# Optimization experiments

Hardware: AMD Instinct MI355X
Metric: run time of the kernel (lower is better)

## Reference

```python
import jax, jax.numpy as jnp
import numpy as np

N_NODES = 50000
N_EDGES = 300000
D = 256  # node/edge feature dim; MLP input = 3*D = 768


def setup_inputs() -> dict:
    key = jax.random.key(0)
    ks = jax.random.split(key, 5)
    x_node = jax.random.normal(ks[0], (N_NODES, D), dtype=jnp.float32)
    x_edge = jax.random.normal(ks[1], (N_EDGES, D), dtype=jnp.float32)
    edge_index = jax.random.randint(ks[2], (2, N_EDGES), 0, N_NODES, dtype=jnp.int64)
    # MLP params: Linear(3*D, D) -> ReLU -> Linear(D, D)
    W1 = jax.random.normal(ks[3], (3 * D, D), dtype=jnp.float32) * (1.0 / np.sqrt(3 * D))
    b1 = jnp.zeros((D,), dtype=jnp.float32)
    W2 = jax.random.normal(ks[4], (D, D), dtype=jnp.float32) * (1.0 / np.sqrt(D))
    b2 = jnp.zeros((D,), dtype=jnp.float32)
    return {"x_node": x_node, "x_edge": x_edge, "edge_index": edge_index,
            "W1": W1, "b1": b1, "W2": W2, "b2": b2}


def reference(x_node, x_edge, edge_index, W1, b1, W2, b2):
    # gather src/dst node feats and concat with edge feats: [E, 3*D]
    src = x_node[edge_index[0]]
    dst = x_node[edge_index[1]]
    h = jnp.concatenate([src, dst, x_edge], axis=1)
    # MLP (custom_func): Linear -> ReLU -> Linear
    h = jax.nn.relu(h @ W1 + b1)
    x_edge_ = h @ W2 + b2
    return x_edge_
```

## Files before the change

### kernel.cpp

```cpp
#include <hip/hip_runtime.h>


typedef __attribute__((ext_vector_type(8))) short short8;
typedef __attribute__((ext_vector_type(4))) float f32x4;
typedef __attribute__((address_space(1))) unsigned int* gp1_t;
typedef __attribute__((address_space(3))) unsigned int* lp3_t;

#define LDO 260

__device__ __forceinline__ unsigned short f2b(float f) {
  unsigned int u = __float_as_uint(f);
  return (unsigned short)((u + 0x7FFFu + ((u >> 16) & 1u)) >> 16);
}
__device__ __forceinline__ unsigned int f2b2(float lo, float hi) {
  return (unsigned int)f2b(lo) | ((unsigned int)f2b(hi) << 16);
}
__device__ __forceinline__ float b2f(unsigned int u) {
  return __uint_as_float((u & 0xffffu) << 16);
}
__device__ __forceinline__ void gload16(const void* g, void* l) {
  __builtin_amdgcn_global_load_lds((gp1_t)g, (lp3_t)l, 16, 0, 0);
}

__global__ void prep_w_kernel(const float* __restrict__ w,
                              unsigned short* __restrict__ wp, int total) {
  int i = blockIdx.x * 256 + threadIdx.x;
  if (i >= total) return;
  int step = i >> 14;
  int rem = i & 16383;
  int n = rem >> 6;
  int s = (rem >> 3) & 7;
  int j = i & 7;
  int k = step * 64 + (((s ^ (n & 7)) << 3) | j);
  wp[i] = f2b(w[(size_t)k * 256 + n]);
}

__global__ __launch_bounds__(512) void node_p_kernel(
    const float* __restrict__ xnode, const unsigned short* __restrict__ wtab,
    unsigned short* __restrict__ Pbase, int NN) {
  __shared__ __align__(16) char smem[65536];

  const int t = threadIdx.x, w = t >> 6, l = t & 63;
  const int lr = l & 15, lk = l >> 4;
  const int wr = w >> 2, wc = w & 3;
  const int nbase = blockIdx.x * 256;
  const char* wt = (const char*)wtab + blockIdx.y * 131072;
  unsigned short* P = Pbase + (size_t)blockIdx.y * NN * 256;

  const int r2 = t >> 1;
  int row2 = nbase + r2;
  if (row2 >= NN) row2 = NN - 1;

  f32x4 acc[8][4];
#pragma unroll
  for (int i = 0; i < 8; ++i)
#pragma unroll
    for (int j = 0; j < 4; ++j) acc[i][j] = (f32x4)0.0f;

  auto stageA = [&](int s, int buf) {
    const int rb = r2 & 7;
    float4 v[8];
#pragma unroll
    for (int jj = 0; jj < 4; ++jj) {
      const int j = (t & 1) * 4 + jj;
      const float* p = xnode + (size_t)row2 * 256 + s * 64 + j * 8;
      v[2 * jj] = ((const float4*)p)[0];
      v[2 * jj + 1] = ((const float4*)p)[1];
    }
#pragma unroll
    for (int jj = 0; jj < 4; ++jj) {
      const int j = (t & 1) * 4 + jj;
      uint4 u;
      u.x = f2b2(v[2 * jj].x, v[2 * jj].y);
      u.y = f2b2(v[2 * jj].z, v[2 * jj].w);
      u.z = f2b2(v[2 * jj + 1].x, v[2 * jj + 1].y);
      u.w = f2b2(v[2 * jj + 1].z, v[2 * jj + 1].w);
      *(uint4*)(smem + buf * 32768 + r2 * 128 + ((j ^ rb) << 4)) = u;
    }
  };

  stageA(0, 0);
  __syncthreads();
  for (int k = 0; k < 4; ++k) {
    if (k + 1 < 4) stageA(k + 1, (k + 1) & 1);
    const char* A = smem + (k & 1) * 32768;
    const char* wb = wt + k * 32768;
    __builtin_amdgcn_s_setprio(1);
#pragma unroll
    for (int ks = 0; ks < 2; ++ks) {
      short8 bf[4];
#pragma unroll
      for (int ni = 0; ni < 4; ++ni) {
        const int n = wc * 64 + ni * 16 + lr;
        bf[ni] = *(const short8*)(wb + n * 128 + (((ks * 4 + lk) ^ (n & 7)) << 4));
      }
#pragma unroll
      for (int mi = 0; mi < 8; ++mi) {
        const int m = wr * 128 + mi * 16 + lr;
        short8 af = *(const short8*)(A + m * 128 + (((ks * 4 + lk) ^ (m & 7)) << 4));
#pragma unroll
        for (int ni = 0; ni < 4; ++ni)
          acc[mi][ni] = __builtin_amdgcn_mfma_f32_16x16x32_bf16(
              af, bf[ni], acc[mi][ni], 0, 0, 0);
      }
    }
    __builtin_amdgcn_s_setprio(0);
    __syncthreads();
  }

#pragma unroll
  for (int mi = 0; mi < 8; ++mi)
#pragma unroll
    for (int r = 0; r < 4; ++r) {
      const int node = nbase + wr * 128 + mi * 16 + lk * 4 + r;
      if (node < NN) {
        uint2 o;
        o.x = f2b2(acc[mi][0][r], acc[mi][1][r]);
        o.y = f2b2(acc[mi][2][r], acc[mi][3][r]);
        *(uint2*)((char*)P + (size_t)node * 512 + lr * 32 + wc * 8) = o;
      }
    }
}

__global__ __launch_bounds__(512) void edge_mlp_p(
    const float* __restrict__ xedge, const int* __restrict__ eidx,
    const unsigned short* __restrict__ Ps, const unsigned short* __restrict__ Pd,
    const unsigned short* __restrict__ wt1ep, const float* __restrict__ b1,
    const unsigned short* __restrict__ wt2p, const float* __restrict__ b2,
    float* __restrict__ out, int E) {
  __shared__ __align__(16) char smem[133120];

  const int t = threadIdx.x, w = t >> 6, l = t & 63;
  const int lr = l & 15, lk = l >> 4;
  const int wr = w >> 2, wc = w & 3;
  const int ebase = blockIdx.x * 256;

  int* sIdx = (int*)(smem + 131072);
  int* dIdx = (int*)(smem + 131072 + 1024);
  {
    const int i = t & 255;
    int e = ebase + i;
    if (e >= E) e = E - 1;
    if (t < 256) sIdx[i] = eidx[e];
    else         dIdx[i] = eidx[(size_t)E + e];
  }

  const int r2 = t >> 1;
  int e2 = ebase + r2;
  if (e2 >= E) e2 = E - 1;

  f32x4 acc[8][4];
#pragma unroll
  for (int i = 0; i < 8; ++i)
#pragma unroll
    for (int j = 0; j < 4; ++j) acc[i][j] = (f32x4)0.0f;

  auto stageB = [&](int step, int buf) {
    const char* g = (const char*)wt1ep + (size_t)step * 32768 + (t << 4);
    char* d = smem + 65536 + buf * 32768 + (w << 10) + (l << 4);
#pragma unroll
    for (int q = 0; q < 4; ++q) gload16(g + q * 8192, d + q * 8192);
  };
  auto stageA = [&](int s, int buf) {
    const int rb = r2 & 7;
    float4 v[8];
#pragma unroll
    for (int jj = 0; jj < 4; ++jj) {
      const int j = (t & 1) * 4 + jj;
      const float* p = xedge + (size_t)e2 * 256 + s * 64 + j * 8;
      v[2 * jj] = ((const float4*)p)[0];
      v[2 * jj + 1] = ((const float4*)p)[1];
    }
#pragma unroll
    for (int jj = 0; jj < 4; ++jj) {
      const int j = (t & 1) * 4 + jj;
      uint4 u;
      u.x = f2b2(v[2 * jj].x, v[2 * jj].y);
      u.y = f2b2(v[2 * jj].z, v[2 * jj].w);
      u.z = f2b2(v[2 * jj + 1].x, v[2 * jj + 1].y);
      u.w = f2b2(v[2 * jj + 1].z, v[2 * jj + 1].w);
      *(uint4*)(smem + buf * 32768 + r2 * 128 + ((j ^ rb) << 4)) = u;
    }
  };
  auto compute = [&](int k) {
    const char* A = smem + (k & 1) * 32768;
    const char* B = smem + 65536 + (k & 1) * 32768;
    __builtin_amdgcn_s_setprio(1);
#pragma unroll
    for (int ks = 0; ks < 2; ++ks) {
      short8 bf[4];
#pragma unroll
      for (int ni = 0; ni < 4; ++ni) {
        const int n = wc * 64 + ni * 16 + lr;
        bf[ni] = *(const short8*)(B + n * 128 + (((ks * 4 + lk) ^ (n & 7)) << 4));
      }
#pragma unroll
      for (int mi = 0; mi < 8; ++mi) {
        const int m = wr * 128 + mi * 16 + lr;
        short8 af = *(const short8*)(A + m * 128 + (((ks * 4 + lk) ^ (m & 7)) << 4));
#pragma unroll
        for (int ni = 0; ni < 4; ++ni)
          acc[mi][ni] = __builtin_amdgcn_mfma_f32_16x16x32_bf16(
              af, bf[ni], acc[mi][ni], 0, 0, 0);
      }
    }
    __builtin_amdgcn_s_setprio(0);
  };

  stageA(0, 0);
  stageB(0, 0);
  __syncthreads();
  for (int k = 0; k < 4; ++k) {
    if (k + 1 < 4) {
      stageB(k + 1, (k + 1) & 1);
      stageA(k + 1, (k + 1) & 1);
    }
    compute(k);
    __syncthreads();
  }

  char* Hs = smem;
  float bias4[4];
#pragma unroll
  for (int ni = 0; ni < 4; ++ni) bias4[ni] = b1[wc * 64 + ni * 16 + lr];
#pragma unroll
  for (int mi = 0; mi < 8; ++mi) {
    uint2 pls[4], pld[4];
#pragma unroll
    for (int r = 0; r < 4; ++r) {
      const int m = wr * 128 + mi * 16 + lk * 4 + r;
      const int si = sIdx[m], di = dIdx[m];
      pls[r] = *(const uint2*)((const char*)Ps + (size_t)si * 512 + lr * 32 + wc * 8);
      pld[r] = *(const uint2*)((const char*)Pd + (size_t)di * 512 + lr * 32 + wc * 8);
    }
#pragma unroll
    for (int ni = 0; ni < 4; ++ni) {
      const int col = wc * 64 + ni * 16 + lr;
      const int cole = col & ~1;
      const int chunk = cole >> 3;
      const int cb = (cole & 6) * 2;
      float v[4], p[4];
#pragma unroll
      for (int r = 0; r < 4; ++r) {
        const unsigned us = (ni < 2) ? (pls[r].x >> (16 * ni)) : (pls[r].y >> (16 * (ni - 2)));
        const unsigned ud = (ni < 2) ? (pld[r].x >> (16 * ni)) : (pld[r].y >> (16 * (ni - 2)));
        float x = acc[mi][ni][r] + bias4[ni] + b2f(us) + b2f(ud);
        v[r] = x > 0.f ? x : 0.f;
        acc[mi][ni][r] = 0.f;
      }
#pragma unroll
      for (int r = 0; r < 4; ++r) p[r] = __shfl_xor(v[r], 1, 64);
      const int r0 = (lr & 1) ? 2 : 0;
#pragma unroll
      for (int rr = 0; rr < 2; ++rr) {
        const int r = r0 + rr;
        const int row = wr * 128 + mi * 16 + lk * 4 + r;
        const float lo = (lr & 1) ? p[r] : v[r];
        const float hi = (lr & 1) ? v[r] : p[r];
        *(unsigned int*)(Hs + row * 512 + ((chunk ^ (row & 7)) << 4) + cb) =
            f2b2(lo, hi);
      }
    }
  }
  __syncthreads();

  short8 bfA[4], bfB[4];
  auto loadB2 = [&](int pair, short8 (&bf)[4]) {
    const char* wb = (const char*)wt2p + (pair >> 1) * 32768;
    const int ksl = (pair & 1) * 4 + lk;
#pragma unroll
    for (int ni = 0; ni < 4; ++ni) {
      const int n = wc * 64 + ni * 16 + lr;
      bf[ni] = *(const short8*)(wb + n * 128 + ((ksl ^ (n & 7)) << 4));
    }
  };
  auto mfmaH = [&](int pair, short8 (&bf)[4]) {
    const int j = (pair >> 1) * 8 + (pair & 1) * 4 + lk;
    __builtin_amdgcn_s_setprio(1);
#pragma unroll
    for (int mi = 0; mi < 8; ++mi) {
      const int m = wr * 128 + mi * 16 + lr;
      short8 af = *(const short8*)(Hs + m * 512 + ((j ^ (m & 7)) << 4));
#pragma unroll
      for (int ni = 0; ni < 4; ++ni)
        acc[mi][ni] = __builtin_amdgcn_mfma_f32_16x16x32_bf16(
            af, bf[ni], acc[mi][ni], 0, 0, 0);
    }
    __builtin_amdgcn_s_setprio(0);
  };
  loadB2(0, bfA);
#pragma unroll
  for (int pair = 0; pair < 8; pair += 2) {
    if (pair + 1 < 8) loadB2(pair + 1, bfB);
    mfmaH(pair, bfA);
    if (pair + 2 < 8) loadB2(pair + 2, bfA);
    if (pair + 1 < 8) mfmaH(pair + 1, bfB);
  }

  float* outst = (float*)smem;
#pragma unroll
  for (int p = 0; p < 4; ++p) {
    __syncthreads();
    if (wr == (p >> 1)) {
#pragma unroll
      for (int ni = 0; ni < 4; ++ni) {
        const int col = wc * 64 + ni * 16 + lr;
        const float bias = b2[col];
#pragma unroll
        for (int mh = 0; mh < 4; ++mh) {
          const int mi = (p & 1) * 4 + mh;
#pragma unroll
          for (int r = 0; r < 4; ++r)
            outst[(mh * 16 + lk * 4 + r) * LDO + col] = acc[mi][ni][r] + bias;
        }
      }
    }
    __syncthreads();
#pragma unroll
    for (int it = 0; it < 8; ++it) {
      const int idx = it * 2048 + t * 4;
      const int lrow = idx >> 8;
      const int cc = idx & 255;
      const int grow = ebase + p * 64 + lrow;
      if (grow < E)
        *(float4*)(out + (size_t)grow * 256 + cc) =
            *(const float4*)(outst + lrow * LDO + cc);
    }
  }
}

__global__ __launch_bounds__(512) void edge_mlp_fb(
    const float* __restrict__ xnode, const float* __restrict__ xedge,
    const int* __restrict__ eidx,
    const unsigned short* __restrict__ wt1p, const float* __restrict__ b1,
    const unsigned short* __restrict__ wt2p, const float* __restrict__ b2,
    float* __restrict__ out, int E) {
  __shared__ __align__(16) char smem[131072];

  const int t = threadIdx.x, w = t >> 6, l = t & 63;
  const int lr = l & 15, lk = l >> 4;
  const int wr = w >> 2, wc = w & 3;
  const int ebase = blockIdx.x * 256;

  const int r2 = t >> 1;
  int e2 = ebase + r2;
  if (e2 >= E) e2 = E - 1;
  const int ns2 = eidx[e2], nd2 = eidx[(size_t)E + e2];

  f32x4 acc[8][4];
#pragma unroll
  for (int i = 0; i < 8; ++i)
#pragma unroll
    for (int j = 0; j < 4; ++j) acc[i][j] = (f32x4)0.0f;

  auto stageB = [&](int step, int buf) {
    const char* g = (const char*)wt1p + (size_t)step * 32768 + (t << 4);
    char* d = smem + 65536 + buf * 32768 + (w << 10) + (l << 4);
#pragma unroll
    for (int q = 0; q < 4; ++q) gload16(g + q * 8192, d + q * 8192);
  };
  auto stageA_f32 = [&](const float* base, int rowid, int coloff, int buf) {
    const int rb = r2 & 7;
    float4 v[8];
#pragma unroll
    for (int jj = 0; jj < 4; ++jj) {
      const int j = (t & 1) * 4 + jj;
      const float* p = base + (size_t)rowid * 256 + coloff + j * 8;
      v[2 * jj] = ((const float4*)p)[0];
      v[2 * jj + 1] = ((const float4*)p)[1];
    }
#pragma unroll
    for (int jj = 0; jj < 4; ++jj) {
      const int j = (t & 1) * 4 + jj;
      uint4 u;
      u.x = f2b2(v[2 * jj].x, v[2 * jj].y);
      u.y = f2b2(v[2 * jj].z, v[2 * jj].w);
      u.z = f2b2(v[2 * jj + 1].x, v[2 * jj + 1].y);
      u.w = f2b2(v[2 * jj + 1].z, v[2 * jj + 1].w);
      *(uint4*)(smem + buf * 32768 + r2 * 128 + ((j ^ rb) << 4)) = u;
    }
  };
  auto stageA = [&](int s, int buf) {
    if (s < 4)       stageA_f32(xnode, ns2, s * 64, buf);
    else if (s < 8)  stageA_f32(xnode, nd2, (s - 4) * 64, buf);
    else             stageA_f32(xedge, e2, (s - 8) * 64, buf);
  };
  auto compute = [&](int k) {
    const char* A = smem + (k & 1) * 32768;
    const char* B = smem + 65536 + (k & 1) * 32768;
    __builtin_amdgcn_s_setprio(1);
#pragma unroll
    for (int ks = 0; ks < 2; ++ks) {
      short8 bf[4];
#pragma unroll
      for (int ni = 0; ni < 4; ++ni) {
        const int n = wc * 64 + ni * 16 + lr;
        bf[ni] = *(const short8*)(B + n * 128 + (((ks * 4 + lk) ^ (n & 7)) << 4));
      }
#pragma unroll
      for (int mi = 0; mi < 8; ++mi) {
        const int m = wr * 128 + mi * 16 + lr;
        short8 af = *(const short8*)(A + m * 128 + (((ks * 4 + lk) ^ (m & 7)) << 4));
#pragma unroll
        for (int ni = 0; ni < 4; ++ni)
          acc[mi][ni] = __builtin_amdgcn_mfma_f32_16x16x32_bf16(
              af, bf[ni], acc[mi][ni], 0, 0, 0);
      }
    }
    __builtin_amdgcn_s_setprio(0);
  };

  stageA(0, 0);
  stageB(0, 0);
  __syncthreads();
  for (int k = 0; k < 12; ++k) {
    if (k + 1 < 12) {
      stageB(k + 1, (k + 1) & 1);
      stageA(k + 1, (k + 1) & 1);
    }
    compute(k);
    __syncthreads();
  }

  char* Hs = smem;
#pragma unroll
  for (int ni = 0; ni < 4; ++ni) {
    const int col = wc * 64 + ni * 16 + lr;
    const float bias = b1[col];
    const int cole = col & ~1;
    const int chunk = cole >> 3;
    const int cb = (cole & 6) * 2;
#pragma unroll
    for (int mi = 0; mi < 8; ++mi) {
      float v[4], p[4];
#pragma unroll
      for (int r = 0; r < 4; ++r) {
        float x = acc[mi][ni][r] + bias;
        v[r] = x > 0.f ? x : 0.f;
        acc[mi][ni][r] = 0.f;
      }
#pragma unroll
      for (int r = 0; r < 4; ++r) p[r] = __shfl_xor(v[r], 1, 64);
      const int r0 = (lr & 1) ? 2 : 0;
#pragma unroll
      for (int rr = 0; rr < 2; ++rr) {
        const int r = r0 + rr;
        const int row = wr * 128 + mi * 16 + lk * 4 + r;
        const float lo = (lr & 1) ? p[r] : v[r];
        const float hi = (lr & 1) ? v[r] : p[r];
        *(unsigned int*)(Hs + row * 512 + ((chunk ^ (row & 7)) << 4) + cb) =
            f2b2(lo, hi);
      }
    }
  }
  __syncthreads();

  short8 bfA[4], bfB[4];
  auto loadB2 = [&](int pair, short8 (&bf)[4]) {
    const char* wb = (const char*)wt2p + (pair >> 1) * 32768;
    const int ksl = (pair & 1) * 4 + lk;
#pragma unroll
    for (int ni = 0; ni < 4; ++ni) {
      const int n = wc * 64 + ni * 16 + lr;
      bf[ni] = *(const short8*)(wb + n * 128 + ((ksl ^ (n & 7)) << 4));
    }
  };
  auto mfmaH = [&](int pair, short8 (&bf)[4]) {
    const int j = (pair >> 1) * 8 + (pair & 1) * 4 + lk;
    __builtin_amdgcn_s_setprio(1);
#pragma unroll
    for (int mi = 0; mi < 8; ++mi) {
      const int m = wr * 128 + mi * 16 + lr;
      short8 af = *(const short8*)(Hs + m * 512 + ((j ^ (m & 7)) << 4));
#pragma unroll
      for (int ni = 0; ni < 4; ++ni)
        acc[mi][ni] = __builtin_amdgcn_mfma_f32_16x16x32_bf16(
            af, bf[ni], acc[mi][ni], 0, 0, 0);
    }
    __builtin_amdgcn_s_setprio(0);
  };
  loadB2(0, bfA);
#pragma unroll
  for (int pair = 0; pair < 8; pair += 2) {
    if (pair + 1 < 8) loadB2(pair + 1, bfB);
    mfmaH(pair, bfA);
    if (pair + 2 < 8) loadB2(pair + 2, bfA);
    if (pair + 1 < 8) mfmaH(pair + 1, bfB);
  }

  float* outst = (float*)smem;
#pragma unroll
  for (int p = 0; p < 4; ++p) {
    __syncthreads();
    if (wr == (p >> 1)) {
#pragma unroll
      for (int ni = 0; ni < 4; ++ni) {
        const int col = wc * 64 + ni * 16 + lr;
        const float bias = b2[col];
#pragma unroll
        for (int mh = 0; mh < 4; ++mh) {
          const int mi = (p & 1) * 4 + mh;
#pragma unroll
          for (int r = 0; r < 4; ++r)
            outst[(mh * 16 + lk * 4 + r) * LDO + col] = acc[mi][ni][r] + bias;
        }
      }
    }
    __syncthreads();
#pragma unroll
    for (int it = 0; it < 8; ++it) {
      const int idx = it * 2048 + t * 4;
      const int lrow = idx >> 8;
      const int cc = idx & 255;
      const int grow = ebase + p * 64 + lrow;
      if (grow < E)
        *(float4*)(out + (size_t)grow * 256 + cc) =
            *(const float4*)(outst + lrow * LDO + cc);
    }
  }
}

extern "C" void kernel_launch(void* const* d_in, const int* in_sizes, int n_in,
                              void* d_out, int out_size, void* d_ws, size_t ws_size,
                              hipStream_t stream) {
  const float* xnode = (const float*)d_in[0];
  const float* xedge = (const float*)d_in[1];
  const int* eidx = (const int*)d_in[2];
  const float* W1 = (const float*)d_in[3];
  const float* b1 = (const float*)d_in[4];
  const float* W2 = (const float*)d_in[5];
  const float* b2 = (const float*)d_in[6];
  float* out = (float*)d_out;

  const int NN = in_sizes[0] / 256;
  const int E = in_sizes[1] / 256;
  const int grid = (E + 255) / 256;

  char* ws = (char*)d_ws;
  const size_t need_new = 4 * 131072 + (size_t)2 * NN * 512;

  if (ws_size >= need_new) {
    unsigned short* wt1sp = (unsigned short*)ws;
    unsigned short* wt1dp = (unsigned short*)(ws + 131072);
    unsigned short* wt1ep = (unsigned short*)(ws + 262144);
    unsigned short* wt2p  = (unsigned short*)(ws + 393216);
    unsigned short* Ps    = (unsigned short*)(ws + 524288);
    unsigned short* Pd    = Ps + (size_t)NN * 256;

    prep_w_kernel<<<256, 256, 0, stream>>>(W1, wt1sp, 65536);
    prep_w_kernel<<<256, 256, 0, stream>>>(W1 + 65536, wt1dp, 65536);
    prep_w_kernel<<<256, 256, 0, stream>>>(W1 + 131072, wt1ep, 65536);
    prep_w_kernel<<<256, 256, 0, stream>>>(W2, wt2p, 65536);

    node_p_kernel<<<dim3((NN + 255) / 256, 2), 512, 0, stream>>>(xnode, wt1sp,
                                                                 Ps, NN);
    edge_mlp_p<<<grid, 512, 0, stream>>>(xedge, eidx, Ps, Pd, wt1ep, b1,
                                         wt2p, b2, out, E);
  } else {
    unsigned short* wt1p = (unsigned short*)ws;
    unsigned short* wt2p = (unsigned short*)(ws + 12 * 32768);
    prep_w_kernel<<<(12 * 16384 + 255) / 256, 256, 0, stream>>>(W1, wt1p,
                                                                12 * 16384);
    prep_w_kernel<<<256, 256, 0, stream>>>(W2, wt2p, 65536);
    edge_mlp_fb<<<grid, 512, 0, stream>>>(xnode, xedge, eidx, wt1p, b1,
                                          wt2p, b2, out, E);
  }
}
```

Before: 385.4 us.

## Shrink edge MLP tiles to 64 edges per block and read W1 directly from global

Replaces the 256-edge, 512-thread edge MLP block with a 64-edge, 256-thread block that uses about 33 KB of LDS, with launch bounds allowing four blocks per CU. W1 edge-part tiles are no longer staged in LDS; each wave loads its B fragments straight from global/L2, as the W2 phase already does. This cuts LDS and accumulator pressure so more blocks can be resident and hide gather and load latency. In exchange, each weight byte is reused across fewer rows per block, so global/L2 weight traffic rises and the output store loop adds extra barriers.

```diff
diff --git a/kernel.cpp b/kernel.cpp
--- a/kernel.cpp
+++ b/kernel.cpp
@@ -122,120 +122,111 @@
     }
 }
 
-__global__ __launch_bounds__(512) void edge_mlp_p(
+__global__ __launch_bounds__(256, 4) void edge_mlp_lite(
     const float* __restrict__ xedge, const int* __restrict__ eidx,
     const unsigned short* __restrict__ Ps, const unsigned short* __restrict__ Pd,
     const unsigned short* __restrict__ wt1ep, const float* __restrict__ b1,
     const unsigned short* __restrict__ wt2p, const float* __restrict__ b2,
     float* __restrict__ out, int E) {
-  __shared__ __align__(16) char smem[133120];
+  __shared__ __align__(16) char smem[33280];
 
   const int t = threadIdx.x, w = t >> 6, l = t & 63;
   const int lr = l & 15, lk = l >> 4;
-  const int wr = w >> 2, wc = w & 3;
-  const int ebase = blockIdx.x * 256;
-
-  int* sIdx = (int*)(smem + 131072);
-  int* dIdx = (int*)(smem + 131072 + 1024);
-  {
-    const int i = t & 255;
+  const int ebase = blockIdx.x * 64;
+
+  int* sIdx = (int*)(smem + 32768);
+  int* dIdx = (int*)(smem + 33024);
+  if (t < 128) {
+    const int i = t & 63;
     int e = ebase + i;
     if (e >= E) e = E - 1;
-    if (t < 256) sIdx[i] = eidx[e];
-    else         dIdx[i] = eidx[(size_t)E + e];
-  }
-
-  const int r2 = t >> 1;
-  int e2 = ebase + r2;
-  if (e2 >= E) e2 = E - 1;
-
-  f32x4 acc[8][4];
-#pragma unroll
-  for (int i = 0; i < 8; ++i)
+    if (t < 64) sIdx[i] = eidx[e];
+    else        dIdx[i] = eidx[(size_t)E + e];
+  }
+
+  const int r4 = t >> 2, q = t & 3;
+  int e4 = ebase + r4;
+  if (e4 >= E) e4 = E - 1;
+
+  f32x4 acc[4][4];
+#pragma unroll
+  for (int i = 0; i < 4; ++i)
 #pragma unroll
     for (int j = 0; j < 4; ++j) acc[i][j] = (f32x4)0.0f;
 
-  auto stageB = [&](int step, int buf) {
-    const char* g = (const char*)wt1ep + (size_t)step * 32768 + (t << 4);
-    char* d = smem + 65536 + buf * 32768 + (w << 10) + (l << 4);
-#pragma unroll
-    for (int q = 0; q < 4; ++q) gload16(g + q * 8192, d + q * 8192);
-  };
   auto stageA = [&](int s, int buf) {
-    const int rb = r2 & 7;
-    float4 v[8];
-#pragma unroll
-    for (int jj = 0; jj < 4; ++jj) {
-      const int j = (t & 1) * 4 + jj;
-      const float* p = xedge + (size_t)e2 * 256 + s * 64 + j * 8;
+    const int rb = r4 & 7;
+    float4 v[4];
+#pragma unroll
+    for (int jj = 0; jj < 2; ++jj) {
+      const int j = 2 * q + jj;
+      const float* p = xedge + (size_t)e4 * 256 + s * 64 + j * 8;
       v[2 * jj] = ((const float4*)p)[0];
       v[2 * jj + 1] = ((const float4*)p)[1];
     }
 #pragma unroll
-    for (int jj = 0; jj < 4; ++jj) {
-      const int j = (t & 1) * 4 + jj;
+    for (int jj = 0; jj < 2; ++jj) {
+      const int j = 2 * q + jj;
       uint4 u;
       u.x = f2b2(v[2 * jj].x, v[2 * jj].y);
       u.y = f2b2(v[2 * jj].z, v[2 * jj].w);
       u.z = f2b2(v[2 * jj + 1].x, v[2 * jj + 1].y);
       u.w = f2b2(v[2 * jj + 1].z, v[2 * jj + 1].w);
-      *(uint4*)(smem + buf * 32768 + r2 * 128 + ((j ^ rb) << 4)) = u;
-    }
-  };
-  auto compute = [&](int k) {
-    const char* A = smem + (k & 1) * 32768;
-    const char* B = smem + 65536 + (k & 1) * 32768;
+      *(uint4*)(smem + buf * 8192 + r4 * 128 + ((j ^ rb) << 4)) = u;
+    }
+  };
+  auto compute1 = [&](int k) {
+    const char* A = smem + (k & 1) * 8192;
+    const char* wb = (const char*)wt1ep + (size_t)k * 32768;
     __builtin_amdgcn_s_setprio(1);
 #pragma unroll
     for (int ks = 0; ks < 2; ++ks) {
-      short8 bf[4];
+      short8 bf[4], af[4];
 #pragma unroll
       for (int ni = 0; ni < 4; ++ni) {
-        const int n = wc * 64 + ni * 16 + lr;
-        bf[ni] = *(const short8*)(B + n * 128 + (((ks * 4 + lk) ^ (n & 7)) << 4));
-      }
-#pragma unroll
-      for (int mi = 0; mi < 8; ++mi) {
-        const int m = wr * 128 + mi * 16 + lr;
-        short8 af = *(const short8*)(A + m * 128 + (((ks * 4 + lk) ^ (m & 7)) << 4));
+        const int n = w * 64 + ni * 16 + lr;
+        bf[ni] = *(const short8*)(wb + n * 128 + (((ks * 4 + lk) ^ (n & 7)) << 4));
+      }
+#pragma unroll
+      for (int mi = 0; mi < 4; ++mi) {
+        const int m = mi * 16 + lr;
+        af[mi] = *(const short8*)(A + m * 128 + (((ks * 4 + lk) ^ (m & 7)) << 4));
+      }
+#pragma unroll
+      for (int mi = 0; mi < 4; ++mi)
 #pragma unroll
         for (int ni = 0; ni < 4; ++ni)
           acc[mi][ni] = __builtin_amdgcn_mfma_f32_16x16x32_bf16(
-              af, bf[ni], acc[mi][ni], 0, 0, 0);
-      }
+              af[mi], bf[ni], acc[mi][ni], 0, 0, 0);
     }
     __builtin_amdgcn_s_setprio(0);
   };
 
   stageA(0, 0);
-  stageB(0, 0);
   __syncthreads();
   for (int k = 0; k < 4; ++k) {
-    if (k + 1 < 4) {
-      stageB(k + 1, (k + 1) & 1);
-      stageA(k + 1, (k + 1) & 1);
-    }
-    compute(k);
+    if (k + 1 < 4) stageA(k + 1, (k + 1) & 1);
+    compute1(k);
     __syncthreads();
   }
 
   char* Hs = smem;
   float bias4[4];
 #pragma unroll
-  for (int ni = 0; ni < 4; ++ni) bias4[ni] = b1[wc * 64 + ni * 16 + lr];
-#pragma unroll
-  for (int mi = 0; mi < 8; ++mi) {
+  for (int ni = 0; ni < 4; ++ni) bias4[ni] = b1[w * 64 + ni * 16 + lr];
+#pragma unroll
+  for (int mi = 0; mi < 4; ++mi) {
     uint2 pls[4], pld[4];
 #pragma unroll
     for (int r = 0; r < 4; ++r) {
-      const int m = wr * 128 + mi * 16 + lk * 4 + r;
+      const int m = mi * 16 + lk * 4 + r;
       const int si = sIdx[m], di = dIdx[m];
-      pls[r] = *(const uint2*)((const char*)Ps + (size_t)si * 512 + lr * 32 + wc * 8);
-      pld[r] = *(const uint2*)((const char*)Pd + (size_t)di * 512 + lr * 32 + wc * 8);
+      pls[r] = *(const uint2*)((const char*)Ps + (size_t)si * 512 + lr * 32 + w * 8);
+      pld[r] = *(const uint2*)((const char*)Pd + (size_t)di * 512 + lr * 32 + w * 8);
     }
 #pragma unroll
     for (int ni = 0; ni < 4; ++ni) {
-      const int col = wc * 64 + ni * 16 + lr;
+      const int col = w * 64 + ni * 16 + lr;
       const int cole = col & ~1;
       const int chunk = cole >> 3;
       const int cb = (cole & 6) * 2;
@@ -254,7 +245,7 @@
 #pragma unroll
       for (int rr = 0; rr < 2; ++rr) {
         const int r = r0 + rr;
-        const int row = wr * 128 + mi * 16 + lk * 4 + r;
+        const int row = mi * 16 + lk * 4 + r;
         const float lo = (lr & 1) ? p[r] : v[r];
         const float hi = (lr & 1) ? v[r] : p[r];
         *(unsigned int*)(Hs + row * 512 + ((chunk ^ (row & 7)) << 4) + cb) =
@@ -266,11 +257,11 @@
 
   short8 bfA[4], bfB[4];
   auto loadB2 = [&](int pair, short8 (&bf)[4]) {
-    const char* wb = (const char*)wt2p + (pair >> 1) * 32768;
+    const char* wb = (const char*)wt2p + (size_t)(pair >> 1) * 32768;
     const int ksl = (pair & 1) * 4 + lk;
 #pragma unroll
     for (int ni = 0; ni < 4; ++ni) {
-      const int n = wc * 64 + ni * 16 + lr;
+      const int n = w * 64 + ni * 16 + lr;
       bf[ni] = *(const short8*)(wb + n * 128 + ((ksl ^ (n & 7)) << 4));
     }
   };
@@ -278,8 +269,8 @@
     const int j = (pair >> 1) * 8 + (pair & 1) * 4 + lk;
     __builtin_amdgcn_s_setprio(1);
 #pragma unroll
-    for (int mi = 0; mi < 8; ++mi) {
-      const int m = wr * 128 + mi * 16 + lr;
+    for (int mi = 0; mi < 4; ++mi) {
+      const int m = mi * 16 + lr;
       short8 af = *(const short8*)(Hs + m * 512 + ((j ^ (m & 7)) << 4));
 #pragma unroll
       for (int ni = 0; ni < 4; ++ni)
@@ -296,36 +287,31 @@
     if (pair + 2 < 8) loadB2(pair + 2, bfA);
     if (pair + 1 < 8) mfmaH(pair + 1, bfB);
   }
+  __syncthreads();
 
   float* outst = (float*)smem;
 #pragma unroll
   for (int p = 0; p < 4; ++p) {
-    __syncthreads();
-    if (wr == (p >> 1)) {
-#pragma unroll
-      for (int ni = 0; ni < 4; ++ni) {
-        const int col = wc * 64 + ni * 16 + lr;
-        const float bias = b2[col];
-#pragma unroll
-        for (int mh = 0; mh < 4; ++mh) {
-          const int mi = (p & 1) * 4 + mh;
-#pragma unroll
-          for (int r = 0; r < 4; ++r)
-            outst[(mh * 16 + lk * 4 + r) * LDO + col] = acc[mi][ni][r] + bias;
-        }
-      }
-    }
-    __syncthreads();
-#pragma unroll
-    for (int it = 0; it < 8; ++it) {
-      const int idx = it * 2048 + t * 4;
+#pragma unroll
+    for (int ni = 0; ni < 4; ++ni) {
+      const int col = w * 64 + ni * 16 + lr;
+      const float bias = b2[col];
+#pragma unroll
+      for (int r = 0; r < 4; ++r)
+        outst[(lk * 4 + r) * LDO + col] = acc[p][ni][r] + bias;
+    }
+    __syncthreads();
+#pragma unroll
+    for (int it = 0; it < 4; ++it) {
+      const int idx = it * 1024 + t * 4;
       const int lrow = idx >> 8;
       const int cc = idx & 255;
-      const int grow = ebase + p * 64 + lrow;
+      const int grow = ebase + p * 16 + lrow;
       if (grow < E)
         *(float4*)(out + (size_t)grow * 256 + cc) =
             *(const float4*)(outst + lrow * LDO + cc);
     }
+    __syncthreads();
   }
 }
 
@@ -534,7 +520,6 @@
 
   const int NN = in_sizes[0] / 256;
   const int E = in_sizes[1] / 256;
-  const int grid = (E + 255) / 256;
 
   char* ws = (char*)d_ws;
   const size_t need_new = 4 * 131072 + (size_t)2 * NN * 512;
@@ -554,15 +539,17 @@
 
     node_p_kernel<<<dim3((NN + 255) / 256, 2), 512, 0, stream>>>(xnode, wt1sp,
                                                                  Ps, NN);
-    edge_mlp_p<<<grid, 512, 0, stream>>>(xedge, eidx, Ps, Pd, wt1ep, b1,
-                                         wt2p, b2, out, E);
+    edge_mlp_lite<<<(E + 63) / 64, 256, 0, stream>>>(xedge, eidx, Ps, Pd,
+                                                     wt1ep, b1, wt2p, b2,
+                                                     out, E);
   } else {
     unsigned short* wt1p = (unsigned short*)ws;
     unsigned short* wt2p = (unsigned short*)(ws + 12 * 32768);
     prep_w_kernel<<<(12 * 16384 + 255) / 256, 256, 0, stream>>>(W1, wt1p,
                                                                 12 * 16384);
     prep_w_kernel<<<256, 256, 0, stream>>>(W2, wt2p, 65536);
-    edge_mlp_fb<<<grid, 512, 0, stream>>>(xnode, xedge, eidx, wt1p, b1,
-                                          wt2p, b2, out, E);
-  }
-}
+    edge_mlp_fb<<<(E + 255) / 256, 512, 0, stream>>>(xnode, xedge, eidx,
+                                                     wt1p, b1, wt2p, b2,
+                                                     out, E);
+  }
+}
```

New measurement: 380.0 us. No clear change (-1.4%).
